# Performance work log

Hardware: AMD Instinct MI355X
Metric: run time of the kernel (lower is better)

Reference implementation:

```python
import jax, jax.numpy as jnp
import numpy as np

EPS = 1e-6
INF = jnp.float32(1e12)
LAM = 1.0    # self.lam in RHD
ALPHA = 0.5  # 'alpha' is undefined in the original buggy forward; standard RHD uses 0.5


def _edt_sq_last(f):
    # Exact 1D squared distance transform along the last axis via min-plus
    # with the parabola cost (i-j)^2. f: [..., n] -> [..., n].
    n = f.shape[-1]
    idx = jnp.arange(n, dtype=f.dtype)
    d2 = (idx[:, None] - idx[None, :]) ** 2  # [n, n]
    return jnp.min(f[..., None, :] + d2, axis=-1)


def edt_sq(mask):
    # Squared Euclidean distance to nearest False pixel (scipy distance_transform_edt**2).
    # mask: bool [B, H, W]. Batched via lax.map to bound the [H, W, W] intermediate.
    f = jnp.where(mask, INF, jnp.float32(0.0))

    def one(fb):  # fb: [H, W]
        g = _edt_sq_last(fb)                 # pass along W
        d2 = _edt_sq_last(g.T).T             # pass along H
        return jnp.minimum(d2, INF)

    d2 = jax.lax.map(one, f)
    # compute_dtm leaves the map at 0 when the foreground mask is empty
    any_fg = jnp.any(mask, axis=(1, 2))
    return jnp.where(any_fg[:, None, None], d2, jnp.float32(0.0))


def setup_inputs() -> dict:
    key = jax.random.key(0)
    k1, k2 = jax.random.split(key)
    B, C, H, W = 8, 2, 512, 512
    logits = jax.random.normal(k1, (B, C, H, W), dtype=jnp.float32)
    outputs = jax.nn.softmax(logits, axis=1)  # module expects softmax results
    lab = jax.random.randint(k2, (B, H, W), 0, 2, dtype=jnp.int32)
    label_batch = jnp.stack([1 - lab, lab], axis=1)  # (B, 2, H, W) one-hot
    return {"outputs": outputs, "label_batch": label_batch}


def reference(outputs, label_batch):
    lab1_i = label_batch[:, 1]                      # (B, H, W) int
    lab1 = lab1_i.astype(outputs.dtype)

    # ---- HD loss (distance maps are constants: computed under no_grad) ----
    gt_d2 = edt_sq(lab1_i > 0)                      # (B, H, W) squared DTM of GT
    seg_d2 = edt_sq(outputs[:, 1] > 0.5)            # squared DTM of thresholded seg
    delta_s = (outputs[:, 1] - lab1) ** 2
    hd_loss = jnp.mean(delta_s * (seg_d2 + gt_d2))

    # ---- Dice loss on foreground channel ----
    score = outputs[:, 1]
    intersect = jnp.sum(score * lab1)
    denom = jnp.sum(score * score) + jnp.sum(lab1 * lab1)
    dice_loss = 1.0 - (2.0 * intersect + EPS) / (denom + EPS)

    # ---- Cross entropy: F.cross_entropy(outputs, label_batch[:,1].long()) ----
    logp = jax.nn.log_softmax(outputs, axis=1)      # (B, 2, H, W)
    picked = jnp.take_along_axis(logp, lab1_i[:, None].astype(jnp.int32), axis=1)[:, 0]
    ce_loss = -jnp.mean(picked)

    return LAM * (ce_loss + dice_loss) + (1.0 - ALPHA) * hd_loss
```

## Files before the change

kernel.cpp:

```cpp
#include <hip/hip_runtime.h>
#include <math.h>
#include <stdint.h>

#define INF_F 1.0e12f
#define NB 8
#define HW 512
#define PLANE (HW*HW)
#define NPIX (NB*PLANE)
#define NBLK (16*16*NB)

__device__ __attribute__((noinline)) int exactRecompute(
    const float* __restrict__ outputs, const int* __restrict__ labels,
    int b, int z, int y, int x)
{
  const int base = (b*2 + 1)*PLANE;
  int m = 0x7fffffff;
  for (int ady = 0; ady < HW; ++ady) {
    if (ady*ady >= m) break;
    for (int sgn = 0; sgn < 2; ++sgn) {
      if (sgn && ady == 0) break;
      const int yy = sgn ? (y - ady) : (y + ady);
      if (yy < 0 || yy >= HW) continue;
      const int rb = base + yy*HW;
      const int a2 = ady*ady;
      for (int t = 0; t < HW; ++t) {
        const int c2 = a2 + t*t;
        if (c2 >= m) break;
        bool hit = false;
        const int xl = x - t, xr = x + t;
        if (xl >= 0)
          hit = (z == 0) ? (labels[rb + xl] <= 0) : !(outputs[rb + xl] > 0.5f);
        if (!hit && xr < HW)
          hit = (z == 0) ? (labels[rb + xr] <= 0) : !(outputs[rb + xr] > 0.5f);
        if (hit) { m = c2; break; }
      }
    }
  }
  return m;
}

__global__ __launch_bounds__(256) void fused_loss(
    const float* __restrict__ outputs, const int* __restrict__ labels,
    double* __restrict__ partials)
{
  __shared__ unsigned short l16[2][48][4];
  __shared__ uint64_t W[2][48];
  __shared__ double wred[4][5];
  const int tid = threadIdx.x;
  const int x0 = blockIdx.x * 32, y0 = blockIdx.y * 32, b = blockIdx.z;
  const int base1 = (b*2 + 1)*PLANE;

  for (int idx = tid; idx < 288; idx += 256) {
    const int z = idx / 144, rem = idx % 144;
    const int row = rem / 3, ch = rem % 3;
    const int yy = y0 - 8 + row;
    const int xs = x0 - 8 + ch*16;
    uint32_t bits = 0;
    if (yy >= 0 && yy < HW) {
      const int rb = base1 + yy*HW;
      if (xs >= 0 && xs + 16 <= HW) {
        if (z == 0) {
          const int4* p = (const int4*)(labels + rb + xs);
          const int4 a = p[0], c = p[1], d = p[2], e = p[3];
          const int v[16] = {a.x,a.y,a.z,a.w, c.x,c.y,c.z,c.w,
                             d.x,d.y,d.z,d.w, e.x,e.y,e.z,e.w};
#pragma unroll
          for (int t = 0; t < 16; ++t) if (v[t] <= 0) bits |= (1u << t);
        } else {
          const float4* p = (const float4*)(outputs + rb + xs);
          const float4 a = p[0], c = p[1], d = p[2], e = p[3];
          const float v[16] = {a.x,a.y,a.z,a.w, c.x,c.y,c.z,c.w,
                               d.x,d.y,d.z,d.w, e.x,e.y,e.z,e.w};
#pragma unroll
          for (int t = 0; t < 16; ++t) if (!(v[t] > 0.5f)) bits |= (1u << t);
        }
      } else {
        for (int t = 0; t < 16; ++t) {
          const int xx = xs + t;
          if (xx < 0 || xx >= HW) continue;
          const bool bg = (z == 0) ? (labels[rb + xx] <= 0)
                                   : !(outputs[rb + xx] > 0.5f);
          if (bg) bits |= (1u << t);
        }
      }
    }
    l16[z][row][ch] = (unsigned short)bits;
  }
  __syncthreads();
  if (tid < 96) {
    const int z = tid / 48, row = tid % 48;
    W[z][row] = (uint64_t)l16[z][row][0]
              | ((uint64_t)l16[z][row][1] << 16)
              | ((uint64_t)l16[z][row][2] << 32);
  }
  __syncthreads();

  const int lx = tid & 31, lyb = tid >> 5;
  const int px = 8 + lx, sh = 63 - px;
  const int x = x0 + lx;
  const int ry0 = 8 + lyb*4;

  float d2m[2][4];
#pragma unroll
  for (int z = 0; z < 2; ++z) {
    const uint64_t* __restrict__ Wz = W[z];
    int rd2[10];
#pragma unroll
    for (int j = 0; j < 10; ++j) {
      const uint64_t w = Wz[ry0 - 3 + j];
      const int dL = __builtin_clzll((w << sh) | 1ull);
      const int dR = __builtin_ctzll((w >> px) | (1ull << 63));
      const int d = min(dL, dR);
      rd2[j] = d*d;
    }
#pragma unroll
    for (int k = 0; k < 4; ++k) {
      int m = rd2[k+3];
      m = min(m, 1 + min(rd2[k+2], rd2[k+4]));
      m = min(m, 4 + min(rd2[k+1], rd2[k+5]));
      m = min(m, 9 + min(rd2[k+0], rd2[k+6]));
      float d2;
      if (__builtin_expect(m > 16, 0)) {
        const int mr = exactRecompute(outputs, labels, b, z, y0 + lyb*4 + k, x);
        d2 = (mr == 0x7fffffff) ? INF_F : (float)mr;
      } else {
        d2 = (float)m;
      }
      d2m[z][k] = d2;
    }
  }

  float part = 0, fI = 0, fP2 = 0, fL = 0, fCE = 0;
#pragma unroll
  for (int k = 0; k < 4; ++k) {
    const int y = y0 + lyb*4 + k;
    const int off = base1 + y*HW + x;
    const float p1  = outputs[off];
    const float p0v = outputs[off - PLANE];
    const int   lv  = labels[off];
    const float labf = (lv > 0) ? 1.0f : 0.0f;
    const float dl = p1 - labf;
    part = fmaf(dl*dl, d2m[0][k] + d2m[1][k], part);
    fI   = fmaf(p1, labf, fI);
    fP2  = fmaf(p1, p1, fP2);
    fL  += labf;
    const float mm  = fmaxf(p0v, p1);
    const float lse = mm + __logf(1.0f + __expf(fminf(p0v, p1) - mm));
    fCE += ((lv > 0) ? p1 : p0v) - lse;
  }

  double s0 = part, s1 = fI, s2 = fP2, s3 = fL, s4 = fCE;
  for (int off = 32; off > 0; off >>= 1) {
    s0 += __shfl_down(s0, off, 64);
    s1 += __shfl_down(s1, off, 64);
    s2 += __shfl_down(s2, off, 64);
    s3 += __shfl_down(s3, off, 64);
    s4 += __shfl_down(s4, off, 64);
  }
  const int w = tid >> 6;
  if ((tid & 63) == 0) {
    wred[w][0] = s0; wred[w][1] = s1; wred[w][2] = s2; wred[w][3] = s3; wred[w][4] = s4;
  }
  __syncthreads();
  if (tid < 5) {
    const int bid = (blockIdx.z*16 + blockIdx.y)*16 + blockIdx.x;
    partials[tid*NBLK + bid] =
        wred[0][tid] + wred[1][tid] + wred[2][tid] + wred[3][tid];
  }
}

__global__ __launch_bounds__(256) void finalize(
    const double* __restrict__ partials, float* __restrict__ out)
{
  __shared__ double wred[4][5];
  const int tid = threadIdx.x;
  double s[5] = {0, 0, 0, 0, 0};
  for (int i = tid; i < NBLK; i += 256) {
#pragma unroll
    for (int q = 0; q < 5; ++q) s[q] += partials[q*NBLK + i];
  }
  for (int off = 32; off > 0; off >>= 1) {
#pragma unroll
    for (int q = 0; q < 5; ++q) s[q] += __shfl_down(s[q], off, 64);
  }
  const int w = tid >> 6;
  if ((tid & 63) == 0) {
#pragma unroll
    for (int q = 0; q < 5; ++q) wred[w][q] = s[q];
  }
  __syncthreads();
  if (tid == 0) {
#pragma unroll
    for (int q = 0; q < 5; ++q) s[q] = wred[0][q] + wred[1][q] + wred[2][q] + wred[3][q];
    const double N = (double)NPIX;
    const double hd   = s[0] / N;
    const double ce   = -(s[4] / N);
    const double dice = 1.0 - (2.0*s[1] + 1e-6) / (s[2] + s[3] + 1e-6);
    out[0] = (float)(ce + dice + 0.5 * hd);
  }
}

extern "C" void kernel_launch(void* const* d_in, const int* in_sizes, int n_in,
                              void* d_out, int out_size, void* d_ws, size_t ws_size,
                              hipStream_t stream)
{
  const float* outputs = (const float*)d_in[0];
  const int*   labels  = (const int*)d_in[1];
  double* partials = (double*)d_ws;

  fused_loss<<<dim3(16, 16, NB), 256, 0, stream>>>(outputs, labels, partials);
  finalize<<<1, 256, 0, stream>>>(partials, (float*)d_out);
}
```

Before: 92.79 us.

## Build bitmasks via wave ballot and fuse finalize using last-block atomic counter

Halo bitmask construction now uses one coalesced scalar load per lane plus a wave ballot, instead of 16-wide vector loads with bit packing and an extra shared-memory merge stage. Block partial reductions move from double to float shuffles. The separate finalize kernel is removed: the last block to finish, found with an atomic counter and thread fences, does the final reduction. This trades a kernel launch for a memset on the stream, and float partial sums slightly change accumulation precision.

```diff
diff --git a/kernel.cpp b/kernel.cpp
--- a/kernel.cpp
+++ b/kernel.cpp
@@ -41,57 +41,34 @@
 
 __global__ __launch_bounds__(256) void fused_loss(
     const float* __restrict__ outputs, const int* __restrict__ labels,
-    double* __restrict__ partials)
+    float* __restrict__ partials, unsigned int* __restrict__ counter,
+    float* __restrict__ out)
 {
-  __shared__ unsigned short l16[2][48][4];
   __shared__ uint64_t W[2][48];
-  __shared__ double wred[4][5];
+  __shared__ float  wredf[4][5];
+  __shared__ double wredd[4][5];
+  __shared__ int lastFlag;
   const int tid = threadIdx.x;
+  const int wave = tid >> 6, lane = tid & 63;
   const int x0 = blockIdx.x * 32, y0 = blockIdx.y * 32, b = blockIdx.z;
   const int base1 = (b*2 + 1)*PLANE;
 
-  for (int idx = tid; idx < 288; idx += 256) {
-    const int z = idx / 144, rem = idx % 144;
-    const int row = rem / 3, ch = rem % 3;
-    const int yy = y0 - 8 + row;
-    const int xs = x0 - 8 + ch*16;
-    uint32_t bits = 0;
-    if (yy >= 0 && yy < HW) {
-      const int rb = base1 + yy*HW;
-      if (xs >= 0 && xs + 16 <= HW) {
-        if (z == 0) {
-          const int4* p = (const int4*)(labels + rb + xs);
-          const int4 a = p[0], c = p[1], d = p[2], e = p[3];
-          const int v[16] = {a.x,a.y,a.z,a.w, c.x,c.y,c.z,c.w,
-                             d.x,d.y,d.z,d.w, e.x,e.y,e.z,e.w};
-#pragma unroll
-          for (int t = 0; t < 16; ++t) if (v[t] <= 0) bits |= (1u << t);
-        } else {
-          const float4* p = (const float4*)(outputs + rb + xs);
-          const float4 a = p[0], c = p[1], d = p[2], e = p[3];
-          const float v[16] = {a.x,a.y,a.z,a.w, c.x,c.y,c.z,c.w,
-                               d.x,d.y,d.z,d.w, e.x,e.y,e.z,e.w};
-#pragma unroll
-          for (int t = 0; t < 16; ++t) if (!(v[t] > 0.5f)) bits |= (1u << t);
-        }
-      } else {
-        for (int t = 0; t < 16; ++t) {
-          const int xx = xs + t;
-          if (xx < 0 || xx >= HW) continue;
-          const bool bg = (z == 0) ? (labels[rb + xx] <= 0)
-                                   : !(outputs[rb + xx] > 0.5f);
-          if (bg) bits |= (1u << t);
-        }
+  {
+    const int z    = wave >> 1;
+    const int row0 = (wave & 1) * 24;
+    const int xx   = x0 - 8 + lane;
+    const bool xok = (lane < 48) && (xx >= 0) && (xx < HW);
+    for (int r = 0; r < 24; ++r) {
+      const int row = row0 + r;
+      const int yy = y0 - 8 + row;
+      bool pred = false;
+      if (xok && yy >= 0 && yy < HW) {
+        const int off = base1 + yy*HW + xx;
+        pred = z ? !(outputs[off] > 0.5f) : (labels[off] <= 0);
       }
+      const uint64_t word = __ballot(pred);
+      if (lane == 0) W[z][row] = word;
     }
-    l16[z][row][ch] = (unsigned short)bits;
-  }
-  __syncthreads();
-  if (tid < 96) {
-    const int z = tid / 48, row = tid % 48;
-    W[z][row] = (uint64_t)l16[z][row][0]
-              | ((uint64_t)l16[z][row][1] << 16)
-              | ((uint64_t)l16[z][row][2] << 32);
   }
   __syncthreads();
 
@@ -130,7 +107,7 @@
     }
   }
 
-  float part = 0, fI = 0, fP2 = 0, fL = 0, fCE = 0;
+  float s0 = 0, s1 = 0, s2 = 0, s3 = 0, s4 = 0;
 #pragma unroll
   for (int k = 0; k < 4; ++k) {
     const int y = y0 + lyb*4 + k;
@@ -140,16 +117,15 @@
     const int   lv  = labels[off];
     const float labf = (lv > 0) ? 1.0f : 0.0f;
     const float dl = p1 - labf;
-    part = fmaf(dl*dl, d2m[0][k] + d2m[1][k], part);
-    fI   = fmaf(p1, labf, fI);
-    fP2  = fmaf(p1, p1, fP2);
-    fL  += labf;
+    s0 = fmaf(dl*dl, d2m[0][k] + d2m[1][k], s0);
+    s1 = fmaf(p1, labf, s1);
+    s2 = fmaf(p1, p1, s2);
+    s3 += labf;
     const float mm  = fmaxf(p0v, p1);
     const float lse = mm + __logf(1.0f + __expf(fminf(p0v, p1) - mm));
-    fCE += ((lv > 0) ? p1 : p0v) - lse;
+    s4 += ((lv > 0) ? p1 : p0v) - lse;
   }
 
-  double s0 = part, s1 = fI, s2 = fP2, s3 = fL, s4 = fCE;
   for (int off = 32; off > 0; off >>= 1) {
     s0 += __shfl_down(s0, off, 64);
     s1 += __shfl_down(s1, off, 64);
@@ -157,46 +133,50 @@
     s3 += __shfl_down(s3, off, 64);
     s4 += __shfl_down(s4, off, 64);
   }
-  const int w = tid >> 6;
-  if ((tid & 63) == 0) {
-    wred[w][0] = s0; wred[w][1] = s1; wred[w][2] = s2; wred[w][3] = s3; wred[w][4] = s4;
+  if (lane == 0) {
+    wredf[wave][0] = s0; wredf[wave][1] = s1; wredf[wave][2] = s2;
+    wredf[wave][3] = s3; wredf[wave][4] = s4;
   }
   __syncthreads();
-  if (tid < 5) {
+
+  if (tid == 0) {
     const int bid = (blockIdx.z*16 + blockIdx.y)*16 + blockIdx.x;
-    partials[tid*NBLK + bid] =
-        wred[0][tid] + wred[1][tid] + wred[2][tid] + wred[3][tid];
-  }
-}
-
-__global__ __launch_bounds__(256) void finalize(
-    const double* __restrict__ partials, float* __restrict__ out)
-{
-  __shared__ double wred[4][5];
-  const int tid = threadIdx.x;
-  double s[5] = {0, 0, 0, 0, 0};
-  for (int i = tid; i < NBLK; i += 256) {
 #pragma unroll
-    for (int q = 0; q < 5; ++q) s[q] += partials[q*NBLK + i];
-  }
-  for (int off = 32; off > 0; off >>= 1) {
-#pragma unroll
-    for (int q = 0; q < 5; ++q) s[q] += __shfl_down(s[q], off, 64);
-  }
-  const int w = tid >> 6;
-  if ((tid & 63) == 0) {
-#pragma unroll
-    for (int q = 0; q < 5; ++q) wred[w][q] = s[q];
+    for (int q = 0; q < 5; ++q)
+      partials[q*NBLK + bid] =
+          wredf[0][q] + wredf[1][q] + wredf[2][q] + wredf[3][q];
+    __threadfence();
+    const unsigned int old = atomicAdd(counter, 1u);
+    lastFlag = (old == (unsigned int)(NBLK - 1));
   }
   __syncthreads();
-  if (tid == 0) {
+
+  if (lastFlag) {
+    __threadfence();
+    double t[5] = {0, 0, 0, 0, 0};
+    for (int i = tid; i < NBLK; i += 256) {
 #pragma unroll
-    for (int q = 0; q < 5; ++q) s[q] = wred[0][q] + wred[1][q] + wred[2][q] + wred[3][q];
-    const double N = (double)NPIX;
-    const double hd   = s[0] / N;
-    const double ce   = -(s[4] / N);
-    const double dice = 1.0 - (2.0*s[1] + 1e-6) / (s[2] + s[3] + 1e-6);
-    out[0] = (float)(ce + dice + 0.5 * hd);
+      for (int q = 0; q < 5; ++q) t[q] += (double)partials[q*NBLK + i];
+    }
+    for (int off = 32; off > 0; off >>= 1) {
+#pragma unroll
+      for (int q = 0; q < 5; ++q) t[q] += __shfl_down(t[q], off, 64);
+    }
+    if (lane == 0) {
+#pragma unroll
+      for (int q = 0; q < 5; ++q) wredd[wave][q] = t[q];
+    }
+    __syncthreads();
+    if (tid == 0) {
+#pragma unroll
+      for (int q = 0; q < 5; ++q)
+        t[q] = wredd[0][q] + wredd[1][q] + wredd[2][q] + wredd[3][q];
+      const double N = (double)NPIX;
+      const double hd   = t[0] / N;
+      const double ce   = -(t[4] / N);
+      const double dice = 1.0 - (2.0*t[1] + 1e-6) / (t[2] + t[3] + 1e-6);
+      out[0] = (float)(ce + dice + 0.5 * hd);
+    }
   }
 }
 
@@ -206,8 +186,10 @@
 {
   const float* outputs = (const float*)d_in[0];
   const int*   labels  = (const int*)d_in[1];
-  double* partials = (double*)d_ws;
+  float* partials = (float*)d_ws;
+  unsigned int* counter = (unsigned int*)((char*)d_ws + 5*NBLK*sizeof(float));
 
-  fused_loss<<<dim3(16, 16, NB), 256, 0, stream>>>(outputs, labels, partials);
-  finalize<<<1, 256, 0, stream>>>(partials, (float*)d_out);
+  hipMemsetAsync(counter, 0, 4, stream);
+  fused_loss<<<dim3(16, 16, NB), 256, 0, stream>>>(outputs, labels,
+                                                   partials, counter, (float*)d_out);
 }
```

Result: slower. 145.5 us (+56.8%).

## Use taller 32x64 tiles, prefetch pixel loads, drop packing pass, float partials

Applied to the files above, without the earlier changes.

Doubles tile height so each thread handles 8 rows, which cuts the halo-row overhead per output pixel and halves the block count. Pixel loads are issued before the distance computation so their latency overlaps the bit-mask work. The separate 16-bit to 64-bit packing step and its barrier are removed by writing 16-bit chunks straight into the 64-bit shared words. Block reductions switch from double to float, which lowers reduction cost but adds some precision risk in the partial sums.

```diff
diff --git a/kernel.cpp b/kernel.cpp
--- a/kernel.cpp
+++ b/kernel.cpp
@@ -7,7 +7,12 @@
 #define HW 512
 #define PLANE (HW*HW)
 #define NPIX (NB*PLANE)
-#define NBLK (16*16*NB)
+#define TW 32
+#define TH 64
+#define GX (HW/TW)
+#define GY (HW/TH)
+#define NBLK (GX*GY*NB)
+#define WROWS (TH + 16)
 
 __device__ __attribute__((noinline)) int exactRecompute(
     const float* __restrict__ outputs, const int* __restrict__ labels,
@@ -41,22 +46,23 @@
 
 __global__ __launch_bounds__(256) void fused_loss(
     const float* __restrict__ outputs, const int* __restrict__ labels,
-    double* __restrict__ partials)
-{
-  __shared__ unsigned short l16[2][48][4];
-  __shared__ uint64_t W[2][48];
-  __shared__ double wred[4][5];
+    float* __restrict__ partials)
+{
+  __shared__ uint64_t W[2][WROWS];
+  __shared__ float wredf[4][5];
   const int tid = threadIdx.x;
-  const int x0 = blockIdx.x * 32, y0 = blockIdx.y * 32, b = blockIdx.z;
+  const int wave = tid >> 6, lane = tid & 63;
+  const int x0 = blockIdx.x * TW, y0 = blockIdx.y * TH, b = blockIdx.z;
   const int base1 = (b*2 + 1)*PLANE;
 
-  for (int idx = tid; idx < 288; idx += 256) {
-    const int z = idx / 144, rem = idx % 144;
-    const int row = rem / 3, ch = rem % 3;
+  for (int idx = tid; idx < 2*WROWS*4; idx += 256) {
+    const int z   = idx / (WROWS*4);
+    const int rem = idx - z*(WROWS*4);
+    const int row = rem >> 2, ch = rem & 3;
     const int yy = y0 - 8 + row;
     const int xs = x0 - 8 + ch*16;
     uint32_t bits = 0;
-    if (yy >= 0 && yy < HW) {
+    if (ch < 3 && yy >= 0 && yy < HW) {
       const int rb = base1 + yy*HW;
       if (xs >= 0 && xs + 16 <= HW) {
         if (z == 0) {
@@ -84,72 +90,71 @@
         }
       }
     }
-    l16[z][row][ch] = (unsigned short)bits;
+    ((unsigned short*)W)[idx] = (unsigned short)bits;
   }
   __syncthreads();
-  if (tid < 96) {
-    const int z = tid / 48, row = tid % 48;
-    W[z][row] = (uint64_t)l16[z][row][0]
-              | ((uint64_t)l16[z][row][1] << 16)
-              | ((uint64_t)l16[z][row][2] << 32);
-  }
-  __syncthreads();
-
-  const int lx = tid & 31, lyb = tid >> 5;
+
+  const int lx = tid & 31, rg = tid >> 5;
+  const int x = x0 + lx;
+  const int ybase = y0 + rg*8;
+  const int ry0 = 8 + rg*8;
+  float p1v[8], p0v[8]; int lvv[8];
+#pragma unroll
+  for (int k = 0; k < 8; ++k) {
+    const int off = base1 + (ybase + k)*HW + x;
+    p1v[k] = outputs[off];
+    p0v[k] = outputs[off - PLANE];
+    lvv[k] = labels[off];
+  }
+
   const int px = 8 + lx, sh = 63 - px;
-  const int x = x0 + lx;
-  const int ry0 = 8 + lyb*4;
-
-  float d2m[2][4];
+  float d2sum[8];
+#pragma unroll
+  for (int k = 0; k < 8; ++k) d2sum[k] = 0.0f;
 #pragma unroll
   for (int z = 0; z < 2; ++z) {
-    const uint64_t* __restrict__ Wz = W[z];
-    int rd2[10];
-#pragma unroll
-    for (int j = 0; j < 10; ++j) {
-      const uint64_t w = Wz[ry0 - 3 + j];
+    int rd2[14];
+#pragma unroll
+    for (int j = 0; j < 14; ++j) {
+      const uint64_t w = W[z][ry0 - 3 + j];
       const int dL = __builtin_clzll((w << sh) | 1ull);
       const int dR = __builtin_ctzll((w >> px) | (1ull << 63));
       const int d = min(dL, dR);
       rd2[j] = d*d;
     }
 #pragma unroll
-    for (int k = 0; k < 4; ++k) {
+    for (int k = 0; k < 8; ++k) {
       int m = rd2[k+3];
       m = min(m, 1 + min(rd2[k+2], rd2[k+4]));
       m = min(m, 4 + min(rd2[k+1], rd2[k+5]));
       m = min(m, 9 + min(rd2[k+0], rd2[k+6]));
       float d2;
       if (__builtin_expect(m > 16, 0)) {
-        const int mr = exactRecompute(outputs, labels, b, z, y0 + lyb*4 + k, x);
+        const int mr = exactRecompute(outputs, labels, b, z, ybase + k, x);
         d2 = (mr == 0x7fffffff) ? INF_F : (float)mr;
       } else {
         d2 = (float)m;
       }
-      d2m[z][k] = d2;
-    }
-  }
-
-  float part = 0, fI = 0, fP2 = 0, fL = 0, fCE = 0;
-#pragma unroll
-  for (int k = 0; k < 4; ++k) {
-    const int y = y0 + lyb*4 + k;
-    const int off = base1 + y*HW + x;
-    const float p1  = outputs[off];
-    const float p0v = outputs[off - PLANE];
-    const int   lv  = labels[off];
-    const float labf = (lv > 0) ? 1.0f : 0.0f;
+      d2sum[k] += d2;
+    }
+  }
+
+  float s0 = 0, s1 = 0, s2 = 0, s3 = 0, s4 = 0;
+#pragma unroll
+  for (int k = 0; k < 8; ++k) {
+    const float p1  = p1v[k];
+    const float p0f = p0v[k];
+    const float labf = (lvv[k] > 0) ? 1.0f : 0.0f;
     const float dl = p1 - labf;
-    part = fmaf(dl*dl, d2m[0][k] + d2m[1][k], part);
-    fI   = fmaf(p1, labf, fI);
-    fP2  = fmaf(p1, p1, fP2);
-    fL  += labf;
-    const float mm  = fmaxf(p0v, p1);
-    const float lse = mm + __logf(1.0f + __expf(fminf(p0v, p1) - mm));
-    fCE += ((lv > 0) ? p1 : p0v) - lse;
-  }
-
-  double s0 = part, s1 = fI, s2 = fP2, s3 = fL, s4 = fCE;
+    s0 = fmaf(dl*dl, d2sum[k], s0);
+    s1 = fmaf(p1, labf, s1);
+    s2 = fmaf(p1, p1, s2);
+    s3 += labf;
+    const float mm  = fmaxf(p0f, p1);
+    const float lse = mm + __logf(1.0f + __expf(fminf(p0f, p1) - mm));
+    s4 += ((lvv[k] > 0) ? p1 : p0f) - lse;
+  }
+
   for (int off = 32; off > 0; off >>= 1) {
     s0 += __shfl_down(s0, off, 64);
     s1 += __shfl_down(s1, off, 64);
@@ -157,27 +162,27 @@
     s3 += __shfl_down(s3, off, 64);
     s4 += __shfl_down(s4, off, 64);
   }
-  const int w = tid >> 6;
-  if ((tid & 63) == 0) {
-    wred[w][0] = s0; wred[w][1] = s1; wred[w][2] = s2; wred[w][3] = s3; wred[w][4] = s4;
+  if (lane == 0) {
+    wredf[wave][0] = s0; wredf[wave][1] = s1; wredf[wave][2] = s2;
+    wredf[wave][3] = s3; wredf[wave][4] = s4;
   }
   __syncthreads();
   if (tid < 5) {
-    const int bid = (blockIdx.z*16 + blockIdx.y)*16 + blockIdx.x;
+    const int bid = (blockIdx.z*GY + blockIdx.y)*GX + blockIdx.x;
     partials[tid*NBLK + bid] =
-        wred[0][tid] + wred[1][tid] + wred[2][tid] + wred[3][tid];
+        wredf[0][tid] + wredf[1][tid] + wredf[2][tid] + wredf[3][tid];
   }
 }
 
 __global__ __launch_bounds__(256) void finalize(
-    const double* __restrict__ partials, float* __restrict__ out)
+    const float* __restrict__ partials, float* __restrict__ out)
 {
   __shared__ double wred[4][5];
   const int tid = threadIdx.x;
   double s[5] = {0, 0, 0, 0, 0};
   for (int i = tid; i < NBLK; i += 256) {
 #pragma unroll
-    for (int q = 0; q < 5; ++q) s[q] += partials[q*NBLK + i];
+    for (int q = 0; q < 5; ++q) s[q] += (double)partials[q*NBLK + i];
   }
   for (int off = 32; off > 0; off >>= 1) {
 #pragma unroll
@@ -206,8 +211,8 @@
 {
   const float* outputs = (const float*)d_in[0];
   const int*   labels  = (const int*)d_in[1];
-  double* partials = (double*)d_ws;
-
-  fused_loss<<<dim3(16, 16, NB), 256, 0, stream>>>(outputs, labels, partials);
+  float* partials = (float*)d_ws;
+
+  fused_loss<<<dim3(GX, GY, NB), 256, 0, stream>>>(outputs, labels, partials);
   finalize<<<1, 256, 0, stream>>>(partials, (float*)d_out);
 }
```

Measured after the change: 88.76 us. 4.3% less time.
